# Kernel optimization log

Measured on AMD Instinct MI355X. Metric: run time of the kernel, lower is better.

Reference implementation:

```python
import jax, jax.numpy as jnp
import numpy as np

B, T, V, E, H, L = 32, 128, 32000, 512, 512, 3
EPS = 1e-5


def setup_inputs() -> dict:
    key = jax.random.key(0)
    ks = jax.random.split(key, 6)
    idx = jax.random.randint(ks[0], (B, T), 0, V, dtype=jnp.int32)
    emb = jax.random.normal(ks[1], (V, E), dtype=jnp.float32) * 0.02
    # packed gate weights per layer: columns ordered [forget, input, candidate, output]
    # acting on concat([h_prev, x]) of width H+E (matches torch cat order)
    W = jax.random.normal(ks[2], (L, H + E, 4 * H), dtype=jnp.float32) * (1.0 / np.sqrt(H + E))
    b = jnp.zeros((L, 4 * H), dtype=jnp.float32)
    gamma = jnp.ones((H,), dtype=jnp.float32)
    beta = jnp.zeros((H,), dtype=jnp.float32)
    Wh = jax.random.normal(ks[3], (H, V), dtype=jnp.float32) * 0.02
    bh = jnp.zeros((V,), dtype=jnp.float32)
    return {"idx": idx, "emb": emb, "W": W, "b": b, "gamma": gamma, "beta": beta, "Wh": Wh, "bh": bh}


def _lstm_out(idx, emb, W, b):
    x = emb[idx]                       # [B, T, E]
    h0 = jnp.zeros((L, B, H), dtype=x.dtype)
    c0 = jnp.zeros((L, B, H), dtype=x.dtype)

    def step(carry, x_t):
        h, c = carry                   # each [L, B, H]
        new_h, new_c = [], []
        inp = x_t                      # [B, E]
        for i in range(L):
            concat = jnp.concatenate([h[i], inp], axis=1)      # [B, H+E]
            gates = concat @ W[i] + b[i]                       # [B, 4H]
            f, ig, g, o = jnp.split(gates, 4, axis=1)
            f = jax.nn.sigmoid(f)
            ig = jax.nn.sigmoid(ig)
            g = jnp.tanh(g)
            o = jax.nn.sigmoid(o)
            ci = f * c[i] + ig * g
            hi = o * jnp.tanh(ci)
            new_h.append(hi)
            new_c.append(ci)
            inp = hi
        return (jnp.stack(new_h), jnp.stack(new_c)), inp

    _, outs = jax.lax.scan(step, (h0, c0), jnp.swapaxes(x, 0, 1))  # outs: [T, B, H]
    return jnp.swapaxes(outs, 0, 1)    # [B, T, H]


def reference(idx, emb, W, b, gamma, beta, Wh, bh):
    out = _lstm_out(idx, emb, W, b)
    mu = out.mean(-1, keepdims=True)
    var = out.var(-1, keepdims=True)
    out = (out - mu) / jnp.sqrt(var + EPS) * gamma + beta       # LayerNorm
    logits = out @ Wh + bh                                      # [B, T, V]
    return logits
```

## Files before the change

### kernel.cpp

```cpp
#include <hip/hip_runtime.h>

typedef unsigned short u16;
typedef unsigned int u32;
typedef __attribute__((ext_vector_type(8))) __bf16 bf16x8;
typedef __attribute__((ext_vector_type(4))) float f32x4;

#define B_ 32
#define T_ 128
#define V_ 32000
#define H_ 512
#define L_ 3
#define LW 64

__device__ __forceinline__ u16 f2bf(float x) {
  union { float f; u32 u; } v; v.f = x;
  u32 r = v.u + 0x7fffu + ((v.u >> 16) & 1u);
  return (u16)(r >> 16);
}
__device__ __forceinline__ float b2f(u16 h) {
  union { u32 u; float f; } v; v.u = ((u32)h) << 16; return v.f;
}
__device__ __forceinline__ float sigf(float x) { return 1.f / (1.f + __expf(-x)); }
__device__ __forceinline__ float tanhf_(float x) { return 2.f / (1.f + __expf(-2.f * x)) - 1.f; }

__device__ __forceinline__ void gload16(const void* g, void* l) {
  __builtin_amdgcn_global_load_lds((const __attribute__((address_space(1))) u32*)g,
                                   (__attribute__((address_space(3))) u32*)l, 16, 0, 0);
}

union F4B8 { f32x4 f; bf16x8 b; uint4 u; };

__device__ __forceinline__ void load16_sc1(const void* p, F4B8* dst) {
  asm volatile("global_load_dwordx4 %0, %1, off sc1" : "=v"(dst->f) : "v"(p));
}
__device__ __forceinline__ void store_short_sc1(void* p, u32 v) {
  asm volatile("global_store_short %0, %1, off sc1" :: "v"(p), "v"(v));
}

__device__ __forceinline__ bool frags_dirty(const F4B8* r) {
  u32 acc = 0;
#pragma unroll
  for (int i = 0; i < 16; ++i) acc |= r[i].u.x | r[i].u.y | r[i].u.z | r[i].u.w;
  return __ballot((acc & 0x40004000u) != 0u) != 0ull;
}

__global__ __launch_bounds__(64) void k_embed(const int* __restrict__ idx,
                                              const float* __restrict__ emb,
                                              u16* __restrict__ X) {
  int bt = blockIdx.x;
  int b = bt >> 7, t = bt & 127;
  int v = idx[bt];
  const float* src = emb + (size_t)v * H_;
  u16* dst = X + ((size_t)t * B_ + b) * H_;
  int l8 = threadIdx.x << 3;
  float4 f0 = *(const float4*)(src + l8);
  float4 f1 = *(const float4*)(src + l8 + 4);
  uint4 o;
  o.x = (u32)f2bf(f0.x) | ((u32)f2bf(f0.y) << 16);
  o.y = (u32)f2bf(f0.z) | ((u32)f2bf(f0.w) << 16);
  o.z = (u32)f2bf(f1.x) | ((u32)f2bf(f1.y) << 16);
  o.w = (u32)f2bf(f1.z) | ((u32)f2bf(f1.w) << 16);
  *(uint4*)(dst + l8) = o;
}

__global__ __launch_bounds__(256) void k_transpose(const float* __restrict__ Wh,
                                                   u16* __restrict__ WhT) {
  __shared__ u16 tile[64][66];
  int nb = blockIdx.x % 500, kb = blockIdx.x / 500;
  int n0 = nb << 6, k0 = kb << 6;
  int tid = threadIdx.x;
#pragma unroll
  for (int it = 0; it < 16; ++it) {
    int k = (it << 2) + (tid >> 6);
    int n = tid & 63;
    tile[k][n] = f2bf(Wh[(size_t)(k0 + k) * V_ + n0 + n]);
  }
  __syncthreads();
#pragma unroll
  for (int it = 0; it < 16; ++it) {
    int n = (it << 2) + (tid >> 6);
    int k = tid & 63;
    WhT[(size_t)(n0 + n) * H_ + k0 + k] = tile[k][n];
  }
}

__global__ __launch_bounds__(128, 1) void k_lstm(const float* __restrict__ Wg,
                                                 const float* __restrict__ bias,
                                                 const u16* __restrict__ X,
                                                 u16* __restrict__ Hbuf) {
  __shared__ u16 bfrag[32][2][64][8];
  const int l = blockIdx.x / LW, g = blockIdx.x % LW;
  const int tid = threadIdx.x, wave = tid >> 6, lane = tid & 63;

  const float* Wl = Wg + (size_t)l * 1024 * 2048;
  for (int f = tid; f < 4096; f += 128) {
    int kb = f >> 7, nt = (f >> 6) & 1, ln = f & 63;
    int n = (nt << 4) + (ln & 15);
    int col = ((n >> 3) << 9) + (g << 3) + (n & 7);
    int k0 = (kb << 5) + ((ln >> 4) << 3);
#pragma unroll
    for (int j = 0; j < 8; ++j)
      bfrag[kb][nt][ln][j] = f2bf(Wl[(size_t)(k0 + j) * 2048 + col]);
  }
  __syncthreads();
  bf16x8 wfh[16][2], wfx[16][2];
#pragma unroll
  for (int kb = 0; kb < 16; ++kb) {
    wfh[kb][0] = *(const bf16x8*)&bfrag[kb][0][lane][0];
    wfh[kb][1] = *(const bf16x8*)&bfrag[kb][1][lane][0];
    wfx[kb][0] = *(const bf16x8*)&bfrag[16 + kb][0][lane][0];
    wfx[kb][1] = *(const bf16x8*)&bfrag[16 + kb][1][lane][0];
  }

  const int jj = lane & 7, cg = (g << 3) + jj;
  const float bF = bias[l * 2048 + cg];
  const float bI = bias[l * 2048 + 512 + cg];
  const float bG = bias[l * 2048 + 1024 + cg];
  const float bO = bias[l * 2048 + 1536 + cg];
  float cst[4] = {0.f, 0.f, 0.f, 0.f};

  const size_t slice = (size_t)B_ * H_;
  u16* Hl = Hbuf + (size_t)l * (T_ + 1) * slice;
  const u16* inb = (l == 0) ? X : (Hbuf + (size_t)(l - 1) * (T_ + 1) * slice + slice);

  const int mrow = (wave << 4) + (lane & 15);
  const int koff = ((lane >> 4) << 3);

  f32x4 z = {0.f, 0.f, 0.f, 0.f};
  f32x4 pxA0 = z, pxA1 = z, pxB0 = z, pxB1 = z;

  auto do_x = [&](int t) {
    const u16* xin = inb + (size_t)t * slice + (size_t)mrow * H_ + koff;
    F4B8 ax[16];
    if (l == 0) {
#pragma unroll
      for (int kb = 0; kb < 16; ++kb) ax[kb].b = *(const bf16x8*)(xin + (kb << 5));
    } else {
      for (;;) {
#pragma unroll
        for (int kb = 0; kb < 16; ++kb) load16_sc1(xin + (kb << 5), &ax[kb]);
        asm volatile("s_waitcnt vmcnt(0)" ::: "memory");
        __builtin_amdgcn_sched_barrier(0);
        if (!frags_dirty(ax)) break;
      }
    }
    pxA0 = z; pxA1 = z; pxB0 = z; pxB1 = z;
#pragma unroll
    for (int kb = 0; kb < 16; kb += 2) {
      pxA0 = __builtin_amdgcn_mfma_f32_16x16x32_bf16(ax[kb].b, wfx[kb][0], pxA0, 0, 0, 0);
      pxA1 = __builtin_amdgcn_mfma_f32_16x16x32_bf16(ax[kb].b, wfx[kb][1], pxA1, 0, 0, 0);
      pxB0 = __builtin_amdgcn_mfma_f32_16x16x32_bf16(ax[kb + 1].b, wfx[kb + 1][0], pxB0, 0, 0, 0);
      pxB1 = __builtin_amdgcn_mfma_f32_16x16x32_bf16(ax[kb + 1].b, wfx[kb + 1][1], pxB1, 0, 0, 0);
    }
  };

  do_x(0);

  for (int t = 0; t < T_; ++t) {
    f32x4 hA0 = z, hA1 = z, hB0 = z, hB1 = z;
    f32x4 hC0 = z, hC1 = z, hD0 = z, hD1 = z;
    if (t > 0) {
      const u16* hin = Hl + (size_t)t * slice + (size_t)mrow * H_ + koff;
      F4B8 ah[16];
      for (;;) {
#pragma unroll
        for (int kb = 0; kb < 16; ++kb) load16_sc1(hin + (kb << 5), &ah[kb]);
        asm volatile("s_waitcnt vmcnt(0)" ::: "memory");
        __builtin_amdgcn_sched_barrier(0);
        if (!frags_dirty(ah)) break;
      }
#pragma unroll
      for (int kb = 0; kb < 16; kb += 4) {
        hA0 = __builtin_amdgcn_mfma_f32_16x16x32_bf16(ah[kb].b, wfh[kb][0], hA0, 0, 0, 0);
        hA1 = __builtin_amdgcn_mfma_f32_16x16x32_bf16(ah[kb].b, wfh[kb][1], hA1, 0, 0, 0);
        hB0 = __builtin_amdgcn_mfma_f32_16x16x32_bf16(ah[kb + 1].b, wfh[kb + 1][0], hB0, 0, 0, 0);
        hB1 = __builtin_amdgcn_mfma_f32_16x16x32_bf16(ah[kb + 1].b, wfh[kb + 1][1], hB1, 0, 0, 0);
        hC0 = __builtin_amdgcn_mfma_f32_16x16x32_bf16(ah[kb + 2].b, wfh[kb + 2][0], hC0, 0, 0, 0);
        hC1 = __builtin_amdgcn_mfma_f32_16x16x32_bf16(ah[kb + 2].b, wfh[kb + 2][1], hC1, 0, 0, 0);
        hD0 = __builtin_amdgcn_mfma_f32_16x16x32_bf16(ah[kb + 3].b, wfh[kb + 3][0], hD0, 0, 0, 0);
        hD1 = __builtin_amdgcn_mfma_f32_16x16x32_bf16(ah[kb + 3].b, wfh[kb + 3][1], hD1, 0, 0, 0);
      }
    }
    {
      f32x4 s0, s1, q0, q1;
#pragma unroll
      for (int r = 0; r < 4; ++r) {
        s0[r] = pxA0[r] + pxB0[r] + ((hA0[r] + hB0[r]) + (hC0[r] + hD0[r]));
        s1[r] = pxA1[r] + pxB1[r] + ((hA1[r] + hB1[r]) + (hC1[r] + hD1[r]));
      }
#pragma unroll
      for (int r = 0; r < 4; ++r) { q0[r] = __shfl_xor(s0[r], 8); q1[r] = __shfl_xor(s1[r], 8); }
      const bool lo = (lane & 8) == 0;
      float hv[4];
#pragma unroll
      for (int r = 0; r < 4; ++r) {
        float fr = lo ? s0[r] : q0[r];
        float ir = lo ? q0[r] : s0[r];
        float gr = lo ? s1[r] : q1[r];
        float orr = lo ? q1[r] : s1[r];
        float cc = sigf(fr + bF) * cst[r] + sigf(ir + bI) * tanhf_(gr + bG);
        cst[r] = cc;
        hv[r] = sigf(orr + bO) * tanhf_(cc);
      }
      if (lo) {
        int rbase = (wave << 4) + ((lane >> 4) << 2);
        u16* hp = Hl + (size_t)(t + 1) * slice + cg;
#pragma unroll
        for (int r = 0; r < 4; ++r)
          store_short_sc1(hp + (size_t)(rbase + r) * H_, (u32)f2bf(hv[r]));
      }
    }
    if (t + 1 < T_) do_x(t + 1);
  }
}

__global__ __launch_bounds__(64) void k_ln(const u16* __restrict__ H2,
                                           const float* __restrict__ gamma,
                                           const float* __restrict__ beta,
                                           u16* __restrict__ Aln) {
  int bt = blockIdx.x;
  int b = bt >> 7, t = bt & 127;
  const u16* src = H2 + ((size_t)(t + 1) * B_ + b) * H_;
  int l8 = threadIdx.x << 3;
  uint4 r = *(const uint4*)(src + l8);
  float v[8];
  v[0] = b2f(r.x & 0xffff); v[1] = b2f(r.x >> 16);
  v[2] = b2f(r.y & 0xffff); v[3] = b2f(r.y >> 16);
  v[4] = b2f(r.z & 0xffff); v[5] = b2f(r.z >> 16);
  v[6] = b2f(r.w & 0xffff); v[7] = b2f(r.w >> 16);
  float s = 0.f, sq = 0.f;
#pragma unroll
  for (int i = 0; i < 8; ++i) { s += v[i]; sq += v[i] * v[i]; }
#pragma unroll
  for (int off = 32; off > 0; off >>= 1) {
    s += __shfl_xor(s, off);
    sq += __shfl_xor(sq, off);
  }
  float mu = s * (1.f / 512.f);
  float inv = rsqrtf(sq * (1.f / 512.f) - mu * mu + 1e-5f);
  float4 g0 = *(const float4*)(gamma + l8), g1 = *(const float4*)(gamma + l8 + 4);
  float4 be0 = *(const float4*)(beta + l8), be1 = *(const float4*)(beta + l8 + 4);
  float gg[8] = {g0.x, g0.y, g0.z, g0.w, g1.x, g1.y, g1.z, g1.w};
  float bb[8] = {be0.x, be0.y, be0.z, be0.w, be1.x, be1.y, be1.z, be1.w};
  u16 o16[8];
#pragma unroll
  for (int i = 0; i < 8; ++i) o16[i] = f2bf((v[i] - mu) * inv * gg[i] + bb[i]);
  uint4 o;
  o.x = (u32)o16[0] | ((u32)o16[1] << 16);
  o.y = (u32)o16[2] | ((u32)o16[3] << 16);
  o.z = (u32)o16[4] | ((u32)o16[5] << 16);
  o.w = (u32)o16[6] | ((u32)o16[7] << 16);
  *(uint4*)(Aln + (size_t)bt * H_ + l8) = o;
}

__global__ __launch_bounds__(512, 2) void k_gemm(const u16* __restrict__ A,
                                                 const u16* __restrict__ Bt,
                                                 const float* __restrict__ bh,
                                                 float* __restrict__ C) {
  __shared__ u16 As[3][256 * 32];
  __shared__ u16 Bs[3][256 * 32];
  const int tid = threadIdx.x, wave = tid >> 6, lane = tid & 63;
  const int mb = blockIdx.x / 125, nb = blockIdx.x % 125;
  const size_t arow0 = (size_t)mb << 8, bcol0 = (size_t)nb << 8;
  const int wm = wave >> 2, wn = wave & 3;

  const int srow = tid >> 2;
  const int sq = (tid & 3) << 4;
  const int sx = ((srow >> 1) & 3) << 4;
  const int sqg = (sq ^ sx) >> 1;
  const u16* Arow0 = A + (arow0 + srow) * H_ + sqg;
  const u16* Arow1 = A + (arow0 + 128 + srow) * H_ + sqg;
  const u16* Brow0 = Bt + (bcol0 + srow) * H_ + sqg;
  const u16* Brow1 = Bt + (bcol0 + 128 + srow) * H_ + sqg;

  const int rA = lane & 15, kg = lane >> 4;
  const int ko = (((kg << 4) ^ (((rA >> 1) & 3) << 4)) >> 1);

  f32x4 acc[8][4];
  f32x4 z = {0.f, 0.f, 0.f, 0.f};
#pragma unroll
  for (int i = 0; i < 8; ++i)
#pragma unroll
    for (int j = 0; j < 4; ++j) acc[i][j] = z;

  auto stageA = [&](int kt, int c) {
    gload16(Arow0 + (kt << 5), &As[c][wave << 9]);
    gload16(Arow1 + (kt << 5), &As[c][4096 + (wave << 9)]);
  };
  auto stageB = [&](int kt, int c) {
    gload16(Brow0 + (kt << 5), &Bs[c][wave << 9]);
    gload16(Brow1 + (kt << 5), &Bs[c][4096 + (wave << 9)]);
  };

  stageA(0, 0); stageB(0, 0);
  stageA(1, 1); stageB(1, 1);
  asm volatile("s_waitcnt vmcnt(4)" ::: "memory");
  __builtin_amdgcn_s_barrier();

  for (int kt = 0; kt < 16; ++kt) {
    const int c = kt % 3;
    const bool pre = (kt + 2 <= 15);
    const int c2 = (kt + 2) % 3;
    bf16x8 bf[4], af[4];
#pragma unroll
    for (int ni = 0; ni < 4; ++ni)
      bf[ni] = *(const bf16x8*)&Bs[c][((wn << 6) + (ni << 4) + rA) * 32 + ko];
#pragma unroll
    for (int mi = 0; mi < 4; ++mi)
      af[mi] = *(const bf16x8*)&As[c][((wm << 7) + (mi << 4) + rA) * 32 + ko];
    if (pre) stageA(kt + 2, c2);
    __builtin_amdgcn_s_setprio(1);
#pragma unroll
    for (int mi = 0; mi < 4; ++mi)
#pragma unroll
      for (int ni = 0; ni < 4; ++ni)
        acc[mi][ni] = __builtin_amdgcn_mfma_f32_16x16x32_bf16(af[mi], bf[ni], acc[mi][ni], 0, 0, 0);
    __builtin_amdgcn_s_setprio(0);
    bf16x8 af2[4];
#pragma unroll
    for (int mi = 0; mi < 4; ++mi)
      af2[mi] = *(const bf16x8*)&As[c][((wm << 7) + 64 + (mi << 4) + rA) * 32 + ko];
    if (pre) stageB(kt + 2, c2);
    __builtin_amdgcn_s_setprio(1);
#pragma unroll
    for (int mi = 0; mi < 4; ++mi)
#pragma unroll
      for (int ni = 0; ni < 4; ++ni)
        acc[4 + mi][ni] = __builtin_amdgcn_mfma_f32_16x16x32_bf16(af2[mi], bf[ni], acc[4 + mi][ni], 0, 0, 0);
    __builtin_amdgcn_s_setprio(0);
    if (kt < 15) {
      if (pre) {
        asm volatile("s_waitcnt vmcnt(4)" ::: "memory");
      } else {
        asm volatile("s_waitcnt vmcnt(0)" ::: "memory");
      }
      __builtin_amdgcn_sched_barrier(0);
      __builtin_amdgcn_s_barrier();
    }
  }

  const int rb4 = (lane >> 4) << 2, n0 = lane & 15;
#pragma unroll
  for (int ni = 0; ni < 4; ++ni) {
    size_t col = bcol0 + (wn << 6) + (ni << 4) + n0;
    float bv = bh[col];
#pragma unroll
    for (int mi = 0; mi < 8; ++mi) {
      size_t row = arow0 + (wm << 7) + (mi << 4) + rb4;
#pragma unroll
      for (int r = 0; r < 4; ++r)
        C[(row + r) * V_ + col] = acc[mi][ni][r] + bv;
    }
  }
}

extern "C" void kernel_launch(void* const* d_in, const int* in_sizes, int n_in,
                              void* d_out, int out_size, void* d_ws, size_t ws_size,
                              hipStream_t stream) {
  const int* idx = (const int*)d_in[0];
  const float* emb = (const float*)d_in[1];
  const float* Wg = (const float*)d_in[2];
  const float* bias = (const float*)d_in[3];
  const float* gamma = (const float*)d_in[4];
  const float* beta = (const float*)d_in[5];
  const float* Wh = (const float*)d_in[6];
  const float* bh = (const float*)d_in[7];
  float* out = (float*)d_out;

  char* ws = (char*)d_ws;
  const size_t szX = (size_t)T_ * B_ * H_ * 2;
  const size_t szH = (size_t)L_ * (T_ + 1) * B_ * H_ * 2;
  const size_t szA = (size_t)B_ * T_ * H_ * 2;
  const size_t szW = (size_t)V_ * H_ * 2;
  u16* X = (u16*)ws;
  u16* Hbuf = (u16*)(ws + szX);
  u16* Aln = (u16*)(ws + szX + szH);
  u16* WhT = (u16*)(ws + szX + szH + szA);
  if (ws_size < szX + szH + szA + szW) return;

  const size_t slice = (size_t)B_ * H_;
  hipMemsetAsync(Hbuf, 0xFF, szH, stream);
  for (int l = 0; l < L_; ++l)
    hipMemsetAsync(Hbuf + (size_t)l * (T_ + 1) * slice, 0, slice * 2, stream);
  k_embed<<<B_ * T_, 64, 0, stream>>>(idx, emb, X);
  k_transpose<<<500 * 8, 256, 0, stream>>>(Wh, WhT);
  k_lstm<<<L_ * LW, 128, 0, stream>>>(Wg, bias, X, Hbuf);
  k_ln<<<B_ * T_, 64, 0, stream>>>(Hbuf + (size_t)2 * (T_ + 1) * B_ * H_, gamma, beta, Aln);
  k_gemm<<<16 * 125, 512, 0, stream>>>(Aln, WhT, bh, out);
}
```

Baseline: 732.1 us.

## Specialize LSTM waves: one wave does recurrence, other precomputes input projection

The two waves per block now have separate roles. Wave 0 holds the recurrent weights and computes the h-projection and gate math for all 32 batch rows. Wave 1 holds the input weights and computes the next step's x-projection into a double-buffered LDS tile, so that work comes off the serial critical path. This adds a block barrier every timestep and doubles the per-wave recurrent MFMA and load work on the critical wave.

```diff
diff --git a/kernel.cpp b/kernel.cpp
--- a/kernel.cpp
+++ b/kernel.cpp
@@ -37,10 +37,10 @@
   asm volatile("global_store_short %0, %1, off sc1" :: "v"(p), "v"(v));
 }
 
-__device__ __forceinline__ bool frags_dirty(const F4B8* r) {
+__device__ __forceinline__ bool frags_dirty32(const F4B8* r) {
   u32 acc = 0;
 #pragma unroll
-  for (int i = 0; i < 16; ++i) acc |= r[i].u.x | r[i].u.y | r[i].u.z | r[i].u.w;
+  for (int i = 0; i < 32; ++i) acc |= r[i].u.x | r[i].u.y | r[i].u.z | r[i].u.w;
   return __ballot((acc & 0x40004000u) != 0u) != 0ull;
 }
 
@@ -88,7 +88,10 @@
                                                  const float* __restrict__ bias,
                                                  const u16* __restrict__ X,
                                                  u16* __restrict__ Hbuf) {
-  __shared__ u16 bfrag[32][2][64][8];
+  __shared__ char smem[65536];
+  u16 (*bfrag)[2][64][8] = (u16 (*)[2][64][8])smem;
+  float (*px)[32][33] = (float (*)[32][33])smem;
+
   const int l = blockIdx.x / LW, g = blockIdx.x % LW;
   const int tid = threadIdx.x, wave = tid >> 6, lane = tid & 63;
 
@@ -103,114 +106,139 @@
       bfrag[kb][nt][ln][j] = f2bf(Wl[(size_t)(k0 + j) * 2048 + col]);
   }
   __syncthreads();
-  bf16x8 wfh[16][2], wfx[16][2];
+  bf16x8 wf[16][2];
 #pragma unroll
   for (int kb = 0; kb < 16; ++kb) {
-    wfh[kb][0] = *(const bf16x8*)&bfrag[kb][0][lane][0];
-    wfh[kb][1] = *(const bf16x8*)&bfrag[kb][1][lane][0];
-    wfx[kb][0] = *(const bf16x8*)&bfrag[16 + kb][0][lane][0];
-    wfx[kb][1] = *(const bf16x8*)&bfrag[16 + kb][1][lane][0];
-  }
+    int src = (wave == 0) ? kb : 16 + kb;
+    wf[kb][0] = *(const bf16x8*)&bfrag[src][0][lane][0];
+    wf[kb][1] = *(const bf16x8*)&bfrag[src][1][lane][0];
+  }
+  __syncthreads();
 
   const int jj = lane & 7, cg = (g << 3) + jj;
   const float bF = bias[l * 2048 + cg];
   const float bI = bias[l * 2048 + 512 + cg];
   const float bG = bias[l * 2048 + 1024 + cg];
   const float bO = bias[l * 2048 + 1536 + cg];
-  float cst[4] = {0.f, 0.f, 0.f, 0.f};
+  float cst[2][4] = {{0.f, 0.f, 0.f, 0.f}, {0.f, 0.f, 0.f, 0.f}};
 
   const size_t slice = (size_t)B_ * H_;
   u16* Hl = Hbuf + (size_t)l * (T_ + 1) * slice;
   const u16* inb = (l == 0) ? X : (Hbuf + (size_t)(l - 1) * (T_ + 1) * slice + slice);
 
-  const int mrow = (wave << 4) + (lane & 15);
-  const int koff = ((lane >> 4) << 3);
+  const int arow = lane & 15;
+  const int koff = (lane >> 4) << 3;
+  const int rb = (lane >> 4) << 2;
+  const int n0 = lane & 15;
 
   f32x4 z = {0.f, 0.f, 0.f, 0.f};
-  f32x4 pxA0 = z, pxA1 = z, pxB0 = z, pxB1 = z;
-
-  auto do_x = [&](int t) {
-    const u16* xin = inb + (size_t)t * slice + (size_t)mrow * H_ + koff;
-    F4B8 ax[16];
+
+  auto x_into_lds = [&](int t, int buf) {
+    const u16* xb = inb + (size_t)t * slice;
+    F4B8 ax[32];
     if (l == 0) {
 #pragma unroll
-      for (int kb = 0; kb < 16; ++kb) ax[kb].b = *(const bf16x8*)(xin + (kb << 5));
+      for (int rg = 0; rg < 2; ++rg)
+#pragma unroll
+        for (int kb = 0; kb < 16; ++kb)
+          ax[rg * 16 + kb].b = *(const bf16x8*)(xb + (size_t)((rg << 4) + arow) * H_ + (kb << 5) + koff);
     } else {
       for (;;) {
 #pragma unroll
-        for (int kb = 0; kb < 16; ++kb) load16_sc1(xin + (kb << 5), &ax[kb]);
+        for (int rg = 0; rg < 2; ++rg)
+#pragma unroll
+          for (int kb = 0; kb < 16; ++kb)
+            load16_sc1(xb + (size_t)((rg << 4) + arow) * H_ + (kb << 5) + koff, &ax[rg * 16 + kb]);
         asm volatile("s_waitcnt vmcnt(0)" ::: "memory");
         __builtin_amdgcn_sched_barrier(0);
-        if (!frags_dirty(ax)) break;
+        if (!frags_dirty32(ax)) break;
       }
     }
-    pxA0 = z; pxA1 = z; pxB0 = z; pxB1 = z;
+    f32x4 a0[2][2] = {{z, z}, {z, z}}, a1[2][2] = {{z, z}, {z, z}};
 #pragma unroll
     for (int kb = 0; kb < 16; kb += 2) {
-      pxA0 = __builtin_amdgcn_mfma_f32_16x16x32_bf16(ax[kb].b, wfx[kb][0], pxA0, 0, 0, 0);
-      pxA1 = __builtin_amdgcn_mfma_f32_16x16x32_bf16(ax[kb].b, wfx[kb][1], pxA1, 0, 0, 0);
-      pxB0 = __builtin_amdgcn_mfma_f32_16x16x32_bf16(ax[kb + 1].b, wfx[kb + 1][0], pxB0, 0, 0, 0);
-      pxB1 = __builtin_amdgcn_mfma_f32_16x16x32_bf16(ax[kb + 1].b, wfx[kb + 1][1], pxB1, 0, 0, 0);
-    }
-  };
-
-  do_x(0);
-
-  for (int t = 0; t < T_; ++t) {
-    f32x4 hA0 = z, hA1 = z, hB0 = z, hB1 = z;
-    f32x4 hC0 = z, hC1 = z, hD0 = z, hD1 = z;
-    if (t > 0) {
-      const u16* hin = Hl + (size_t)t * slice + (size_t)mrow * H_ + koff;
-      F4B8 ah[16];
-      for (;;) {
-#pragma unroll
-        for (int kb = 0; kb < 16; ++kb) load16_sc1(hin + (kb << 5), &ah[kb]);
-        asm volatile("s_waitcnt vmcnt(0)" ::: "memory");
-        __builtin_amdgcn_sched_barrier(0);
-        if (!frags_dirty(ah)) break;
-      }
-#pragma unroll
-      for (int kb = 0; kb < 16; kb += 4) {
-        hA0 = __builtin_amdgcn_mfma_f32_16x16x32_bf16(ah[kb].b, wfh[kb][0], hA0, 0, 0, 0);
-        hA1 = __builtin_amdgcn_mfma_f32_16x16x32_bf16(ah[kb].b, wfh[kb][1], hA1, 0, 0, 0);
-        hB0 = __builtin_amdgcn_mfma_f32_16x16x32_bf16(ah[kb + 1].b, wfh[kb + 1][0], hB0, 0, 0, 0);
-        hB1 = __builtin_amdgcn_mfma_f32_16x16x32_bf16(ah[kb + 1].b, wfh[kb + 1][1], hB1, 0, 0, 0);
-        hC0 = __builtin_amdgcn_mfma_f32_16x16x32_bf16(ah[kb + 2].b, wfh[kb + 2][0], hC0, 0, 0, 0);
-        hC1 = __builtin_amdgcn_mfma_f32_16x16x32_bf16(ah[kb + 2].b, wfh[kb + 2][1], hC1, 0, 0, 0);
-        hD0 = __builtin_amdgcn_mfma_f32_16x16x32_bf16(ah[kb + 3].b, wfh[kb + 3][0], hD0, 0, 0, 0);
-        hD1 = __builtin_amdgcn_mfma_f32_16x16x32_bf16(ah[kb + 3].b, wfh[kb + 3][1], hD1, 0, 0, 0);
+#pragma unroll
+      for (int rg = 0; rg < 2; ++rg) {
+        a0[rg][0] = __builtin_amdgcn_mfma_f32_16x16x32_bf16(ax[rg * 16 + kb].b, wf[kb][0], a0[rg][0], 0, 0, 0);
+        a0[rg][1] = __builtin_amdgcn_mfma_f32_16x16x32_bf16(ax[rg * 16 + kb].b, wf[kb][1], a0[rg][1], 0, 0, 0);
+        a1[rg][0] = __builtin_amdgcn_mfma_f32_16x16x32_bf16(ax[rg * 16 + kb + 1].b, wf[kb + 1][0], a1[rg][0], 0, 0, 0);
+        a1[rg][1] = __builtin_amdgcn_mfma_f32_16x16x32_bf16(ax[rg * 16 + kb + 1].b, wf[kb + 1][1], a1[rg][1], 0, 0, 0);
       }
     }
-    {
-      f32x4 s0, s1, q0, q1;
-#pragma unroll
-      for (int r = 0; r < 4; ++r) {
-        s0[r] = pxA0[r] + pxB0[r] + ((hA0[r] + hB0[r]) + (hC0[r] + hD0[r]));
-        s1[r] = pxA1[r] + pxB1[r] + ((hA1[r] + hB1[r]) + (hC1[r] + hD1[r]));
+#pragma unroll
+    for (int rg = 0; rg < 2; ++rg)
+#pragma unroll
+      for (int nt = 0; nt < 2; ++nt)
+#pragma unroll
+        for (int r = 0; r < 4; ++r)
+          px[buf][(rg << 4) + rb + r][(nt << 4) + n0] = a0[rg][nt][r] + a1[rg][nt][r];
+  };
+
+  if (wave == 1) x_into_lds(0, 0);
+  __syncthreads();
+
+  for (int t = 0; t < T_; ++t) {
+    if (wave == 0) {
+      f32x4 a0[2][2] = {{z, z}, {z, z}}, a1[2][2] = {{z, z}, {z, z}};
+      if (t > 0) {
+        const u16* hb = Hl + (size_t)t * slice;
+        F4B8 ah[32];
+        for (;;) {
+#pragma unroll
+          for (int rg = 0; rg < 2; ++rg)
+#pragma unroll
+            for (int kb = 0; kb < 16; ++kb)
+              load16_sc1(hb + (size_t)((rg << 4) + arow) * H_ + (kb << 5) + koff, &ah[rg * 16 + kb]);
+          asm volatile("s_waitcnt vmcnt(0)" ::: "memory");
+          __builtin_amdgcn_sched_barrier(0);
+          if (!frags_dirty32(ah)) break;
+        }
+#pragma unroll
+        for (int kb = 0; kb < 16; kb += 2) {
+#pragma unroll
+          for (int rg = 0; rg < 2; ++rg) {
+            a0[rg][0] = __builtin_amdgcn_mfma_f32_16x16x32_bf16(ah[rg * 16 + kb].b, wf[kb][0], a0[rg][0], 0, 0, 0);
+            a0[rg][1] = __builtin_amdgcn_mfma_f32_16x16x32_bf16(ah[rg * 16 + kb].b, wf[kb][1], a0[rg][1], 0, 0, 0);
+            a1[rg][0] = __builtin_amdgcn_mfma_f32_16x16x32_bf16(ah[rg * 16 + kb + 1].b, wf[kb + 1][0], a1[rg][0], 0, 0, 0);
+            a1[rg][1] = __builtin_amdgcn_mfma_f32_16x16x32_bf16(ah[rg * 16 + kb + 1].b, wf[kb + 1][1], a1[rg][1], 0, 0, 0);
+          }
+        }
       }
-#pragma unroll
-      for (int r = 0; r < 4; ++r) { q0[r] = __shfl_xor(s0[r], 8); q1[r] = __shfl_xor(s1[r], 8); }
-      const bool lo = (lane & 8) == 0;
-      float hv[4];
-#pragma unroll
-      for (int r = 0; r < 4; ++r) {
-        float fr = lo ? s0[r] : q0[r];
-        float ir = lo ? q0[r] : s0[r];
-        float gr = lo ? s1[r] : q1[r];
-        float orr = lo ? q1[r] : s1[r];
-        float cc = sigf(fr + bF) * cst[r] + sigf(ir + bI) * tanhf_(gr + bG);
-        cst[r] = cc;
-        hv[r] = sigf(orr + bO) * tanhf_(cc);
+      const int buf = t & 1;
+#pragma unroll
+      for (int rg = 0; rg < 2; ++rg) {
+        f32x4 s0, s1, q0, q1;
+#pragma unroll
+        for (int r = 0; r < 4; ++r) {
+          s0[r] = a0[rg][0][r] + a1[rg][0][r] + px[buf][(rg << 4) + rb + r][n0];
+          s1[r] = a0[rg][1][r] + a1[rg][1][r] + px[buf][(rg << 4) + rb + r][16 + n0];
+        }
+#pragma unroll
+        for (int r = 0; r < 4; ++r) { q0[r] = __shfl_xor(s0[r], 8); q1[r] = __shfl_xor(s1[r], 8); }
+        const bool lo = (lane & 8) == 0;
+        float hv[4];
+#pragma unroll
+        for (int r = 0; r < 4; ++r) {
+          float fr = lo ? s0[r] : q0[r];
+          float ir = lo ? q0[r] : s0[r];
+          float gr = lo ? s1[r] : q1[r];
+          float orr = lo ? q1[r] : s1[r];
+          float cc = sigf(fr + bF) * cst[rg][r] + sigf(ir + bI) * tanhf_(gr + bG);
+          cst[rg][r] = cc;
+          hv[r] = sigf(orr + bO) * tanhf_(cc);
+        }
+        if (lo) {
+          int rbase = (rg << 4) + rb;
+          u16* hp = Hl + (size_t)(t + 1) * slice + cg;
+#pragma unroll
+          for (int r = 0; r < 4; ++r)
+            store_short_sc1(hp + (size_t)(rbase + r) * H_, (u32)f2bf(hv[r]));
+        }
       }
-      if (lo) {
-        int rbase = (wave << 4) + ((lane >> 4) << 2);
-        u16* hp = Hl + (size_t)(t + 1) * slice + cg;
-#pragma unroll
-        for (int r = 0; r < 4; ++r)
-          store_short_sc1(hp + (size_t)(rbase + r) * H_, (u32)f2bf(hv[r]));
-      }
+    } else {
+      if (t + 1 < T_) x_into_lds(t + 1, (t + 1) & 1);
     }
-    if (t + 1 < T_) do_x(t + 1);
+    __syncthreads();
   }
 }
 
```

After: 985.6 us. 34.6% more time.
